# Kernel optimization log

Measured on AMD Instinct MI355X. Metric: run time of the kernel, lower is better.

Reference implementation:

```python
import jax, jax.numpy as jnp
import numpy as np

B, S, D, H = 64, 2048, 512, 512


def setup_inputs() -> dict:
    key = jax.random.key(0)
    ks = jax.random.split(key, 8)
    return {
        "hidden": jax.random.normal(ks[0], (B, D), dtype=jnp.float32),
        "context": jax.random.normal(ks[1], (B, S, D), dtype=jnp.float32),
        "mask": jax.random.randint(ks[2], (B, S), 0, 2).astype(bool),
        "Wd": jax.random.normal(ks[3], (H, D), dtype=jnp.float32) * 0.05,
        "bd": jax.random.normal(ks[4], (H,), dtype=jnp.float32) * 0.05,
        "We": jax.random.normal(ks[5], (H, D), dtype=jnp.float32) * 0.05,
        "be": jax.random.normal(ks[6], (H,), dtype=jnp.float32) * 0.05,
        "V": jax.random.normal(ks[7], (H,), dtype=jnp.float32) * 0.05,
    }


def reference(hidden, context, mask, Wd, bd, We, be, V):
    # di = d_linear(hidden): [B, H]
    di = hidden @ Wd.T + bd
    # ei = e_linear(context): [B, S, H]
    ei = jnp.einsum("bsd,hd->bsh", context, We) + be
    # additive score u_i = V . tanh(di + ei): [B, S]
    ui = jnp.einsum("h,bsh->bs", V, jnp.tanh(di[:, None, :] + ei))
    # masked positions get -inf (ui[mask] = -inf)
    ui = jnp.where(mask, -jnp.inf, ui)
    alpha = jax.nn.softmax(ui, axis=-1)  # [B, S]
    # context aggregation uses the PROJECTED context ei (as in torch code)
    attention_hidden_state = jnp.einsum("bsh,bs->bh", ei, alpha)
    return alpha, attention_hidden_state
```

## Files before the change

kernel.cpp:

```cpp
#include <hip/hip_runtime.h>
#include <cstdint>

#define B_ 64
#define S_ 2048
#define D_ 512
#define H_ 512

using f32x4  = __attribute__((ext_vector_type(4))) float;
using bf16x8 = __attribute__((ext_vector_type(8))) short;

__device__ __forceinline__ unsigned short f2bf(float f) {
  unsigned u = __float_as_uint(f);
  u += 0x7FFFu + ((u >> 16) & 1u);
  return (unsigned short)(u >> 16);
}
__device__ __forceinline__ unsigned int cvtpk(float lo, float hi) {
  unsigned int r;
  asm("v_cvt_pk_bf16_f32 %0, %1, %2" : "=v"(r) : "v"(lo), "v"(hi));
  return r;
}
__device__ __forceinline__ bf16x8 cvt8(f32x4 a, f32x4 b) {
  union { unsigned int u[4]; bf16x8 v; } r;
  r.u[0] = cvtpk(a[0], a[1]); r.u[1] = cvtpk(a[2], a[3]);
  r.u[2] = cvtpk(b[0], b[1]); r.u[3] = cvtpk(b[2], b[3]);
  return r.v;
}
__device__ __forceinline__ float fast_tanh(float x) {
  float t = __builtin_amdgcn_exp2f(x * 2.8853900817779268f);
  return 1.0f - 2.0f * __builtin_amdgcn_rcpf(t + 1.0f);
}

__device__ __forceinline__ void gl_lds16g(const void* g, void* l) {
  __builtin_amdgcn_global_load_lds(
      (const __attribute__((address_space(1))) unsigned int*)g,
      (__attribute__((address_space(3))) unsigned int*)l, 16, 0, 0);
}

__device__ __forceinline__ void barrier_raw() {
  asm volatile("" ::: "memory");
  __builtin_amdgcn_s_barrier();
  asm volatile("" ::: "memory");
}

__global__ void k_prep(const float* __restrict__ hidden, const float* __restrict__ Wd,
                       const float* __restrict__ bd, float* __restrict__ di,
                       const float* __restrict__ We, unsigned short* __restrict__ Web) {
  if (blockIdx.x < 128) {
    int idx = blockIdx.x * 256 + threadIdx.x;
    int h = idx >> 6;
    int b = idx & 63;
    const f32x4* hp = (const f32x4*)(hidden + (size_t)b * D_);
    const f32x4* wp = (const f32x4*)(Wd + (size_t)h * D_);
    float acc = 0.f;
#pragma unroll 8
    for (int i = 0; i < D_ / 4; ++i) {
      f32x4 x = hp[i], y = wp[i];
      acc += x[0] * y[0] + x[1] * y[1] + x[2] * y[2] + x[3] * y[3];
    }
    di[b * H_ + h] = acc + bd[h];
  } else {
    int i = (blockIdx.x - 128) * 256 + threadIdx.x;
    const f32x4* p = (const f32x4*)(We + (size_t)i * 8);
    f32x4 a = p[0], b = p[1];
    bf16x8 o;
    o[0] = (short)f2bf(a[0]); o[1] = (short)f2bf(a[1]);
    o[2] = (short)f2bf(a[2]); o[3] = (short)f2bf(a[3]);
    o[4] = (short)f2bf(b[0]); o[5] = (short)f2bf(b[1]);
    o[6] = (short)f2bf(b[2]); o[7] = (short)f2bf(b[3]);
    *(bf16x8*)(Web + (size_t)i * 8) = o;
  }
}

__global__ __launch_bounds__(512, 2) void k_ei_gemm(
    const float* __restrict__ A, const unsigned short* __restrict__ Bw,
    const float* __restrict__ be, const float* __restrict__ V,
    const float* __restrict__ di, float* __restrict__ ui2) {
  __shared__ __align__(16) float ldsA[2][128 * 32];
  __shared__ __align__(16) unsigned short ldsB[2][256 * 32];
  __shared__ float ured[8][64];

  const int bid = blockIdx.x;
  const int swz = (bid & 7) * 256 + (bid >> 3);
  const int row0 = (swz >> 1) << 7;
  const int nt   = swz & 1;
  const int cb   = nt << 8;

  const int t  = threadIdx.x;
  const int l  = t & 63;
  const int w  = t >> 6;
  const int wm = (w >> 2) << 6;
  const int wn = (w & 3) << 6;
  const int lr = l & 15;
  const int lg = l >> 4;

  const float* gA = A + (size_t)(row0 + w * 8 + (l >> 3)) * D_ +
                    (((l & 7) ^ ((l >> 3) & 7)) << 2);
  const unsigned short* gB = Bw + (size_t)(cb + w * 16 + (l >> 2)) * D_ +
                             (((l & 3) ^ ((l >> 3) & 3)) << 3);

#define STAGE(bf, kk) do {                                     \
    const int k0_ = (kk) << 5;                                 \
    gl_lds16g(gA + k0_,            &ldsA[bf][w * 256]);        \
    gl_lds16g(gA + 64 * D_ + k0_,  &ldsA[bf][2048 + w * 256]); \
    gl_lds16g(gB + k0_,            &ldsB[bf][w * 512]);        \
    gl_lds16g(gB + 128 * D_ + k0_, &ldsB[bf][4096 + w * 512]); \
  } while (0)

  const int pa0 = (((2 * lg)     ^ (lr & 7)) << 2);
  const int pa1 = (((2 * lg + 1) ^ (lr & 7)) << 2);
  const int rsB = (lg ^ ((lr >> 1) & 3)) << 3;
  const int arow = (wm + lr) * 32;
  const int brow = (wn + lr) * 32;

  f32x4 acc[4][4];
  const f32x4 z = {0.f, 0.f, 0.f, 0.f};
#pragma unroll
  for (int mi = 0; mi < 4; ++mi)
#pragma unroll
    for (int ni = 0; ni < 4; ++ni) acc[mi][ni] = z;

  STAGE(0, 0);
  STAGE(1, 1);

#pragma unroll
  for (int kt = 0; kt < 16; ++kt) {
    if (kt == 15) asm volatile("s_waitcnt vmcnt(0)" ::: "memory");
    else          asm volatile("s_waitcnt vmcnt(4)" ::: "memory");
    barrier_raw();
    const int bf = kt & 1;

    bf16x8 bq0 = *(const bf16x8*)&ldsB[bf][brow + 0 * 512 + rsB];
    bf16x8 bq1 = *(const bf16x8*)&ldsB[bf][brow + 1 * 512 + rsB];
    bf16x8 bq2 = *(const bf16x8*)&ldsB[bf][brow + 2 * 512 + rsB];
    bf16x8 bq3 = *(const bf16x8*)&ldsB[bf][brow + 3 * 512 + rsB];

    __builtin_amdgcn_s_setprio(1);
    {
      f32x4 r00 = *(const f32x4*)&ldsA[bf][arow + 0 * 512 + pa0];
      f32x4 r01 = *(const f32x4*)&ldsA[bf][arow + 0 * 512 + pa1];
      f32x4 r10 = *(const f32x4*)&ldsA[bf][arow + 1 * 512 + pa0];
      f32x4 r11 = *(const f32x4*)&ldsA[bf][arow + 1 * 512 + pa1];
      bf16x8 af0 = cvt8(r00, r01);
      bf16x8 af1 = cvt8(r10, r11);
      acc[0][0] = __builtin_amdgcn_mfma_f32_16x16x32_bf16(af0, bq0, acc[0][0], 0, 0, 0);
      acc[0][1] = __builtin_amdgcn_mfma_f32_16x16x32_bf16(af0, bq1, acc[0][1], 0, 0, 0);
      acc[0][2] = __builtin_amdgcn_mfma_f32_16x16x32_bf16(af0, bq2, acc[0][2], 0, 0, 0);
      acc[0][3] = __builtin_amdgcn_mfma_f32_16x16x32_bf16(af0, bq3, acc[0][3], 0, 0, 0);
      acc[1][0] = __builtin_amdgcn_mfma_f32_16x16x32_bf16(af1, bq0, acc[1][0], 0, 0, 0);
      acc[1][1] = __builtin_amdgcn_mfma_f32_16x16x32_bf16(af1, bq1, acc[1][1], 0, 0, 0);
      acc[1][2] = __builtin_amdgcn_mfma_f32_16x16x32_bf16(af1, bq2, acc[1][2], 0, 0, 0);
      acc[1][3] = __builtin_amdgcn_mfma_f32_16x16x32_bf16(af1, bq3, acc[1][3], 0, 0, 0);
    }
    {
      f32x4 r20 = *(const f32x4*)&ldsA[bf][arow + 2 * 512 + pa0];
      f32x4 r21 = *(const f32x4*)&ldsA[bf][arow + 2 * 512 + pa1];
      f32x4 r30 = *(const f32x4*)&ldsA[bf][arow + 3 * 512 + pa0];
      f32x4 r31 = *(const f32x4*)&ldsA[bf][arow + 3 * 512 + pa1];
      bf16x8 af2 = cvt8(r20, r21);
      bf16x8 af3 = cvt8(r30, r31);
      acc[2][0] = __builtin_amdgcn_mfma_f32_16x16x32_bf16(af2, bq0, acc[2][0], 0, 0, 0);
      acc[2][1] = __builtin_amdgcn_mfma_f32_16x16x32_bf16(af2, bq1, acc[2][1], 0, 0, 0);
      acc[2][2] = __builtin_amdgcn_mfma_f32_16x16x32_bf16(af2, bq2, acc[2][2], 0, 0, 0);
      acc[2][3] = __builtin_amdgcn_mfma_f32_16x16x32_bf16(af2, bq3, acc[2][3], 0, 0, 0);
      acc[3][0] = __builtin_amdgcn_mfma_f32_16x16x32_bf16(af3, bq0, acc[3][0], 0, 0, 0);
      acc[3][1] = __builtin_amdgcn_mfma_f32_16x16x32_bf16(af3, bq1, acc[3][1], 0, 0, 0);
      acc[3][2] = __builtin_amdgcn_mfma_f32_16x16x32_bf16(af3, bq2, acc[3][2], 0, 0, 0);
      acc[3][3] = __builtin_amdgcn_mfma_f32_16x16x32_bf16(af3, bq3, acc[3][3], 0, 0, 0);
    }
    __builtin_amdgcn_s_setprio(0);

    __builtin_amdgcn_sched_barrier(0);
    barrier_raw();
    if (kt + 2 < 16) STAGE(bf, kt + 2);
  }
#undef STAGE

  const int b = row0 >> 11;
  float uacc[4][4];
#pragma unroll
  for (int mi = 0; mi < 4; ++mi)
#pragma unroll
    for (int j = 0; j < 4; ++j) uacc[mi][j] = 0.f;

#pragma unroll
  for (int ni = 0; ni < 4; ++ni) {
    const int gc = cb + wn + ni * 16 + lr;
    const float vv = V[gc];
    const float base = di[b * H_ + gc] + be[gc];
#pragma unroll
    for (int mi = 0; mi < 4; ++mi)
#pragma unroll
      for (int j = 0; j < 4; ++j)
        uacc[mi][j] += vv * fast_tanh(base + acc[mi][ni][j]);
  }
#pragma unroll
  for (int mi = 0; mi < 4; ++mi)
#pragma unroll
    for (int j = 0; j < 4; ++j) {
      float s = uacc[mi][j];
      s += __shfl_xor(s, 1);
      s += __shfl_xor(s, 2);
      s += __shfl_xor(s, 4);
      s += __shfl_xor(s, 8);
      if (lr == 0) ured[w][mi * 16 + (lg << 2) + j] = s;
    }
  __syncthreads();
  if (t < 128) {
    const int r = t & 63, wr = t >> 6;
    ui2[nt * (B_ * S_) + row0 + wr * 64 + r] =
        ured[wr * 4][r] + ured[wr * 4 + 1][r] + ured[wr * 4 + 2][r] +
        ured[wr * 4 + 3][r];
  }
}

__global__ void k_softmax(const float* __restrict__ ui2, const void* __restrict__ mask,
                          float* __restrict__ alpha) {
  __shared__ float red[4];
  __shared__ int sfl;
  const int b = blockIdx.x, t = threadIdx.x;
  const int l = t & 63, w = t >> 6;

  if (t == 0) sfl = 0;
  const unsigned int* mw = (const unsigned int*)mask;
  unsigned det = (mw[b * 512 + t] | mw[b * 512 + 256 + t]) & 0xFFFFFF00u;
  __syncthreads();
  if (det) atomicOr(&sfl, 1);
  __syncthreads();
  const int fl = sfl;

  float u[8];
#pragma unroll
  for (int i = 0; i < 8; ++i) {
    const int idx = b * S_ + t + i * 256;
    const int msk = fl ? (int)((const unsigned char*)mask)[idx]
                       : ((const int*)mask)[idx];
    const float uv = ui2[idx] + ui2[idx + B_ * S_];
    u[i] = msk ? -__builtin_inff() : uv;
  }

  float mx = u[0];
#pragma unroll
  for (int i = 1; i < 8; ++i) mx = fmaxf(mx, u[i]);
#pragma unroll
  for (int off = 32; off; off >>= 1) mx = fmaxf(mx, __shfl_xor(mx, off));
  if (l == 0) red[w] = mx;
  __syncthreads();
  mx = fmaxf(fmaxf(red[0], red[1]), fmaxf(red[2], red[3]));
  __syncthreads();

  float p[8];
  float s = 0.f;
#pragma unroll
  for (int i = 0; i < 8; ++i) {
    p[i] = __builtin_amdgcn_exp2f((u[i] - mx) * 1.4426950408889634f);
    s += p[i];
  }
#pragma unroll
  for (int off = 32; off; off >>= 1) s += __shfl_xor(s, off);
  if (l == 0) red[w] = s;
  __syncthreads();
  s = red[0] + red[1] + red[2] + red[3];

  const float inv = 1.0f / s;
#pragma unroll
  for (int i = 0; i < 8; ++i) alpha[b * S_ + t + i * 256] = p[i] * inv;
}

__global__ void k_wsum(const float* __restrict__ ctx, const float* __restrict__ alpha,
                       float* __restrict__ part) {
  __shared__ float red[3][512];
  const int b = blockIdx.x >> 4, chunk = blockIdx.x & 15;
  const int t = threadIdx.x;
  const int h0 = (t & 63) << 3;
  const int sw = t >> 6;
  const int s0 = chunk << 7;

  float acc[8] = {0.f, 0.f, 0.f, 0.f, 0.f, 0.f, 0.f, 0.f};
#pragma unroll 2
  for (int k = 0; k < 32; ++k) {
    const int s = s0 + sw + (k << 2);
    const float a = alpha[b * S_ + s];
    const f32x4* e = (const f32x4*)(ctx + ((size_t)(b * S_ + s)) * D_ + h0);
    f32x4 e0 = e[0], e1 = e[1];
#pragma unroll
    for (int j = 0; j < 4; ++j) acc[j] += a * e0[j];
#pragma unroll
    for (int j = 0; j < 4; ++j) acc[4 + j] += a * e1[j];
  }
  if (sw) {
#pragma unroll
    for (int j = 0; j < 8; ++j) red[sw - 1][h0 + j] = acc[j];
  }
  __syncthreads();
  if (sw == 0) {
#pragma unroll
    for (int j = 0; j < 8; ++j)
      part[((chunk << 6) + b) * 512 + h0 + j] =
          acc[j] + red[0][h0 + j] + red[1][h0 + j] + red[2][h0 + j];
  }
}

__global__ void k_tail(const float* __restrict__ part, const float* __restrict__ We,
                       const float* __restrict__ be, float* __restrict__ out1) {
  __shared__ float wsum_s[512];
  const int b = blockIdx.x, t = threadIdx.x;

  float s = 0.f;
#pragma unroll
  for (int c = 0; c < 16; ++c) s += part[((c << 6) + b) * 512 + t];
  wsum_s[t] = s;
  __syncthreads();

  const f32x4* wp = (const f32x4*)wsum_s;
  const f32x4* ep = (const f32x4*)(We + (size_t)t * D_);
  float acc = 0.f;
#pragma unroll 8
  for (int i = 0; i < D_ / 4; ++i) {
    f32x4 x = wp[i], y = ep[i];
    acc += x[0] * y[0] + x[1] * y[1] + x[2] * y[2] + x[3] * y[3];
  }
  out1[b * H_ + t] = acc + be[t];
}

extern "C" void kernel_launch(void* const* d_in, const int* in_sizes, int n_in,
                              void* d_out, int out_size, void* d_ws, size_t ws_size,
                              hipStream_t stream) {
  const float* hidden = (const float*)d_in[0];
  const float* ctx    = (const float*)d_in[1];
  const void*  mask   = d_in[2];
  const float* Wd     = (const float*)d_in[3];
  const float* bd     = (const float*)d_in[4];
  const float* We     = (const float*)d_in[5];
  const float* be     = (const float*)d_in[6];
  const float* V      = (const float*)d_in[7];

  float* out   = (float*)d_out;
  float* alpha = out;
  float* out1  = out + B_ * S_;

  char* ws = (char*)d_ws;
  const size_t off_u2  = 0;
  const size_t off_r3  = off_u2 + 4ull * B_ * S_ * 4;
  const size_t off_web = off_r3 + (size_t)B_ * H_ * 4;

  float* ui2  = (float*)(ws + off_u2);
  float* part = (float*)(ws + off_u2);
  float* di   = (float*)(ws + off_r3);
  unsigned short* Web = (unsigned short*)(ws + off_web);

  k_prep<<<256, 256, 0, stream>>>(hidden, Wd, bd, di, We, Web);
  k_ei_gemm<<<(B_ * S_ / 128) * 2, 512, 0, stream>>>(ctx, Web, be, V, di, ui2);
  k_softmax<<<B_, 256, 0, stream>>>(ui2, mask, alpha);
  k_wsum<<<B_ * 16, 256, 0, stream>>>(ctx, alpha, part);
  k_tail<<<B_, 512, 0, stream>>>(part, We, be, out1);
}
```

Before: 205.4 us.

## Enlarge GEMM tile to 256 rows, convert A to bf16 once via registers into LDS

Doubles the per-block M tile from 128 to 256 rows and uses a K step of 64. A is now loaded from global memory into registers, converted to bf16 once and written to LDS, instead of being DMA'd as fp32 and converted by every wave on each read. The main loop is restructured into explicit double-buffered phases with many barriers and manual waitcnt control. This halves redundant A conversion and LDS footprint per element and raises reuse of B. In exchange, register pressure rises sharply with 32 accumulators plus 8 staged vectors, occupancy may drop, and the grid shrinks to half as many blocks.

```diff
diff --git a/kernel.cpp b/kernel.cpp
--- a/kernel.cpp
+++ b/kernel.cpp
@@ -8,6 +8,7 @@
 
 using f32x4  = __attribute__((ext_vector_type(4))) float;
 using bf16x8 = __attribute__((ext_vector_type(8))) short;
+using u32x2  = __attribute__((ext_vector_type(2))) unsigned int;
 
 __device__ __forceinline__ unsigned short f2bf(float f) {
   unsigned u = __float_as_uint(f);
@@ -18,12 +19,6 @@
   unsigned int r;
   asm("v_cvt_pk_bf16_f32 %0, %1, %2" : "=v"(r) : "v"(lo), "v"(hi));
   return r;
-}
-__device__ __forceinline__ bf16x8 cvt8(f32x4 a, f32x4 b) {
-  union { unsigned int u[4]; bf16x8 v; } r;
-  r.u[0] = cvtpk(a[0], a[1]); r.u[1] = cvtpk(a[2], a[3]);
-  r.u[2] = cvtpk(b[0], b[1]); r.u[3] = cvtpk(b[2], b[3]);
-  return r.v;
 }
 __device__ __forceinline__ float fast_tanh(float x) {
   float t = __builtin_amdgcn_exp2f(x * 2.8853900817779268f);
@@ -75,110 +70,135 @@
     const float* __restrict__ A, const unsigned short* __restrict__ Bw,
     const float* __restrict__ be, const float* __restrict__ V,
     const float* __restrict__ di, float* __restrict__ ui2) {
-  __shared__ __align__(16) float ldsA[2][128 * 32];
-  __shared__ __align__(16) unsigned short ldsB[2][256 * 32];
-  __shared__ float ured[8][64];
+  __shared__ __align__(16) unsigned short ldsA[2][512 * 32];
+  __shared__ __align__(16) unsigned short ldsB[2][512 * 32];
+  __shared__ float ured[8][128];
 
   const int bid = blockIdx.x;
-  const int swz = (bid & 7) * 256 + (bid >> 3);
-  const int row0 = (swz >> 1) << 7;
+  const int swz = (bid & 7) * 128 + (bid >> 3);
+  const int row0 = (swz >> 1) << 8;
   const int nt   = swz & 1;
   const int cb   = nt << 8;
 
   const int t  = threadIdx.x;
   const int l  = t & 63;
   const int w  = t >> 6;
-  const int wm = (w >> 2) << 6;
+  const int wm = (w >> 2) << 7;
   const int wn = (w & 3) << 6;
   const int lr = l & 15;
   const int lg = l >> 4;
 
-  const float* gA = A + (size_t)(row0 + w * 8 + (l >> 3)) * D_ +
-                    (((l & 7) ^ ((l >> 3) & 7)) << 2);
-  const unsigned short* gB = Bw + (size_t)(cb + w * 16 + (l >> 2)) * D_ +
+  const float* gA = A + (size_t)(row0 + (t >> 4)) * D_ + ((t & 15) << 2);
+  const int khw  = lr >> 3;
+  const int physw = ((lr >> 1) & 3) ^ ((2 * w + (lg >> 1)) & 3);
+  const int eA = ((khw << 8) + (w << 2) + lg) * 32 + (physw << 3) + ((lr & 1) << 2);
+  const unsigned short* gB = Bw + (size_t)(cb + 16 * w + (l >> 2)) * D_ +
                              (((l & 3) ^ ((l >> 3) & 3)) << 3);
-
-#define STAGE(bf, kk) do {                                     \
-    const int k0_ = (kk) << 5;                                 \
-    gl_lds16g(gA + k0_,            &ldsA[bf][w * 256]);        \
-    gl_lds16g(gA + 64 * D_ + k0_,  &ldsA[bf][2048 + w * 256]); \
-    gl_lds16g(gB + k0_,            &ldsB[bf][w * 512]);        \
-    gl_lds16g(gB + 128 * D_ + k0_, &ldsB[bf][4096 + w * 512]); \
+  const int rs = (lg ^ ((lr >> 1) & 3)) << 3;
+
+  f32x4 a0, a1, a2, a3, a4, a5, a6, a7;
+  bf16x8 af[4], bq[4];
+
+#define LOADA(kt) do { const float* p_ = gA + (kt) * 64;                 \
+    a0 = *(const f32x4*)(p_);             a1 = *(const f32x4*)(p_ + 16384);  \
+    a2 = *(const f32x4*)(p_ + 2*16384);   a3 = *(const f32x4*)(p_ + 3*16384);\
+    a4 = *(const f32x4*)(p_ + 4*16384);   a5 = *(const f32x4*)(p_ + 5*16384);\
+    a6 = *(const f32x4*)(p_ + 6*16384);   a7 = *(const f32x4*)(p_ + 7*16384);\
   } while (0)
 
-  const int pa0 = (((2 * lg)     ^ (lr & 7)) << 2);
-  const int pa1 = (((2 * lg + 1) ^ (lr & 7)) << 2);
-  const int rsB = (lg ^ ((lr >> 1) & 3)) << 3;
-  const int arow = (wm + lr) * 32;
-  const int brow = (wn + lr) * 32;
-
-  f32x4 acc[4][4];
+#define WR1(Q, AV, BF) do { u32x2 p_ = {cvtpk(AV[0], AV[1]), cvtpk(AV[2], AV[3])}; \
+    *(u32x2*)&ldsA[BF][eA + (Q) * 1024] = p_; } while (0)
+#define WRITEA(BF) do { WR1(0, a0, BF); WR1(1, a1, BF); WR1(2, a2, BF); \
+    WR1(3, a3, BF); WR1(4, a4, BF); WR1(5, a5, BF); WR1(6, a6, BF);     \
+    WR1(7, a7, BF); } while (0)
+
+#define DMAB(BF, kt) do {                                                    \
+    gl_lds16g(gB + (kt) * 64,                 &ldsB[BF][(16 * w) * 32]);       \
+    gl_lds16g(gB + 128 * D_ + (kt) * 64,      &ldsB[BF][(128 + 16 * w) * 32]); \
+    gl_lds16g(gB + (kt) * 64 + 32,            &ldsB[BF][(256 + 16 * w) * 32]); \
+    gl_lds16g(gB + 128 * D_ + (kt) * 64 + 32, &ldsB[BF][(384 + 16 * w) * 32]); \
+  } while (0)
+
+#define READ_BQ(BF, KH) do { _Pragma("unroll") for (int ni = 0; ni < 4; ++ni) \
+    bq[ni] = *(const bf16x8*)&ldsB[BF][((KH) * 256 + wn + ni * 16 + lr) * 32 + rs]; } while (0)
+#define READ_AF(BF, KH, MH) do { _Pragma("unroll") for (int mi = 0; mi < 4; ++mi) \
+    af[mi] = *(const bf16x8*)&ldsA[BF][((KH) * 256 + wm + (MH) * 64 + mi * 16 + lr) * 32 + rs]; } while (0)
+
+#define MFMA16(MH) do {                                                  \
+    __builtin_amdgcn_s_setprio(1);                                       \
+    _Pragma("unroll") for (int mi = 0; mi < 4; ++mi)                     \
+      _Pragma("unroll") for (int ni = 0; ni < 4; ++ni)                   \
+        acc[(MH) * 4 + mi][ni] = __builtin_amdgcn_mfma_f32_16x16x32_bf16(\
+            af[mi], bq[ni], acc[(MH) * 4 + mi][ni], 0, 0, 0);            \
+    __builtin_amdgcn_s_setprio(0);                                       \
+  } while (0)
+
+#define VMW8 asm volatile("s_waitcnt lgkmcnt(0)\n\ts_waitcnt vmcnt(8)" ::: "memory")
+#define VMW0 asm volatile("s_waitcnt lgkmcnt(0)\n\ts_waitcnt vmcnt(0)" ::: "memory")
+
+  f32x4 acc[8][4];
   const f32x4 z = {0.f, 0.f, 0.f, 0.f};
 #pragma unroll
-  for (int mi = 0; mi < 4; ++mi)
+  for (int mi = 0; mi < 8; ++mi)
 #pragma unroll
     for (int ni = 0; ni < 4; ++ni) acc[mi][ni] = z;
 
-  STAGE(0, 0);
-  STAGE(1, 1);
-
-#pragma unroll
-  for (int kt = 0; kt < 16; ++kt) {
-    if (kt == 15) asm volatile("s_waitcnt vmcnt(0)" ::: "memory");
-    else          asm volatile("s_waitcnt vmcnt(4)" ::: "memory");
-    barrier_raw();
-    const int bf = kt & 1;
-
-    bf16x8 bq0 = *(const bf16x8*)&ldsB[bf][brow + 0 * 512 + rsB];
-    bf16x8 bq1 = *(const bf16x8*)&ldsB[bf][brow + 1 * 512 + rsB];
-    bf16x8 bq2 = *(const bf16x8*)&ldsB[bf][brow + 2 * 512 + rsB];
-    bf16x8 bq3 = *(const bf16x8*)&ldsB[bf][brow + 3 * 512 + rsB];
-
-    __builtin_amdgcn_s_setprio(1);
-    {
-      f32x4 r00 = *(const f32x4*)&ldsA[bf][arow + 0 * 512 + pa0];
-      f32x4 r01 = *(const f32x4*)&ldsA[bf][arow + 0 * 512 + pa1];
-      f32x4 r10 = *(const f32x4*)&ldsA[bf][arow + 1 * 512 + pa0];
-      f32x4 r11 = *(const f32x4*)&ldsA[bf][arow + 1 * 512 + pa1];
-      bf16x8 af0 = cvt8(r00, r01);
-      bf16x8 af1 = cvt8(r10, r11);
-      acc[0][0] = __builtin_amdgcn_mfma_f32_16x16x32_bf16(af0, bq0, acc[0][0], 0, 0, 0);
-      acc[0][1] = __builtin_amdgcn_mfma_f32_16x16x32_bf16(af0, bq1, acc[0][1], 0, 0, 0);
-      acc[0][2] = __builtin_amdgcn_mfma_f32_16x16x32_bf16(af0, bq2, acc[0][2], 0, 0, 0);
-      acc[0][3] = __builtin_amdgcn_mfma_f32_16x16x32_bf16(af0, bq3, acc[0][3], 0, 0, 0);
-      acc[1][0] = __builtin_amdgcn_mfma_f32_16x16x32_bf16(af1, bq0, acc[1][0], 0, 0, 0);
-      acc[1][1] = __builtin_amdgcn_mfma_f32_16x16x32_bf16(af1, bq1, acc[1][1], 0, 0, 0);
-      acc[1][2] = __builtin_amdgcn_mfma_f32_16x16x32_bf16(af1, bq2, acc[1][2], 0, 0, 0);
-      acc[1][3] = __builtin_amdgcn_mfma_f32_16x16x32_bf16(af1, bq3, acc[1][3], 0, 0, 0);
-    }
-    {
-      f32x4 r20 = *(const f32x4*)&ldsA[bf][arow + 2 * 512 + pa0];
-      f32x4 r21 = *(const f32x4*)&ldsA[bf][arow + 2 * 512 + pa1];
-      f32x4 r30 = *(const f32x4*)&ldsA[bf][arow + 3 * 512 + pa0];
-      f32x4 r31 = *(const f32x4*)&ldsA[bf][arow + 3 * 512 + pa1];
-      bf16x8 af2 = cvt8(r20, r21);
-      bf16x8 af3 = cvt8(r30, r31);
-      acc[2][0] = __builtin_amdgcn_mfma_f32_16x16x32_bf16(af2, bq0, acc[2][0], 0, 0, 0);
-      acc[2][1] = __builtin_amdgcn_mfma_f32_16x16x32_bf16(af2, bq1, acc[2][1], 0, 0, 0);
-      acc[2][2] = __builtin_amdgcn_mfma_f32_16x16x32_bf16(af2, bq2, acc[2][2], 0, 0, 0);
-      acc[2][3] = __builtin_amdgcn_mfma_f32_16x16x32_bf16(af2, bq3, acc[2][3], 0, 0, 0);
-      acc[3][0] = __builtin_amdgcn_mfma_f32_16x16x32_bf16(af3, bq0, acc[3][0], 0, 0, 0);
-      acc[3][1] = __builtin_amdgcn_mfma_f32_16x16x32_bf16(af3, bq1, acc[3][1], 0, 0, 0);
-      acc[3][2] = __builtin_amdgcn_mfma_f32_16x16x32_bf16(af3, bq2, acc[3][2], 0, 0, 0);
-      acc[3][3] = __builtin_amdgcn_mfma_f32_16x16x32_bf16(af3, bq3, acc[3][3], 0, 0, 0);
-    }
-    __builtin_amdgcn_s_setprio(0);
-
-    __builtin_amdgcn_sched_barrier(0);
-    barrier_raw();
-    if (kt + 2 < 16) STAGE(bf, kt + 2);
-  }
-#undef STAGE
+  LOADA(0);
+  DMAB(0, 0);
+  WRITEA(0);
+  LOADA(1);
+  VMW8;
+  barrier_raw();
+
+#define ITER(I, LASTQ)                                                        \
+  do {                                                                        \
+                     \
+    READ_BQ(0, 0); READ_AF(0, 0, 0);                                          \
+    DMAB(1, 2 * (I) + 1);                                                     \
+    WRITEA(1);                                                                \
+    if (!(LASTQ)) LOADA(2 * (I) + 2);                                         \
+    barrier_raw(); MFMA16(0); barrier_raw();                                  \
+                                                          \
+    READ_AF(0, 0, 1); barrier_raw(); MFMA16(1); barrier_raw();                \
+                                                          \
+    READ_BQ(0, 1); READ_AF(0, 1, 0); barrier_raw(); MFMA16(0); barrier_raw(); \
+                                     \
+    READ_AF(0, 1, 1); barrier_raw(); MFMA16(1);                               \
+    if (LASTQ) { VMW0; } else { VMW8; }                                       \
+    barrier_raw();                                                            \
+                     \
+    READ_BQ(1, 0); READ_AF(1, 0, 0);                                          \
+    if (!(LASTQ)) { DMAB(0, 2 * (I) + 2); WRITEA(0); LOADA(2 * (I) + 3); }    \
+    barrier_raw(); MFMA16(0); barrier_raw();                                  \
+                                                          \
+    READ_AF(1, 0, 1); barrier_raw(); MFMA16(1); barrier_raw();                \
+                                                          \
+    READ_BQ(1, 1); READ_AF(1, 1, 0); barrier_raw(); MFMA16(0); barrier_raw(); \
+                                     \
+    READ_AF(1, 1, 1); barrier_raw(); MFMA16(1);                               \
+    if (LASTQ) { VMW0; } else { VMW8; }                                       \
+    barrier_raw();                                                            \
+  } while (0)
+
+  ITER(0, 0);
+  ITER(1, 0);
+  ITER(2, 0);
+  ITER(3, 1);
+#undef ITER
+#undef LOADA
+#undef WR1
+#undef WRITEA
+#undef DMAB
+#undef READ_BQ
+#undef READ_AF
+#undef MFMA16
+#undef VMW8
+#undef VMW0
 
   const int b = row0 >> 11;
-  float uacc[4][4];
-#pragma unroll
-  for (int mi = 0; mi < 4; ++mi)
+  float uacc[8][4];
+#pragma unroll
+  for (int mi = 0; mi < 8; ++mi)
 #pragma unroll
     for (int j = 0; j < 4; ++j) uacc[mi][j] = 0.f;
 
@@ -188,13 +208,13 @@
     const float vv = V[gc];
     const float base = di[b * H_ + gc] + be[gc];
 #pragma unroll
-    for (int mi = 0; mi < 4; ++mi)
+    for (int mi = 0; mi < 8; ++mi)
 #pragma unroll
       for (int j = 0; j < 4; ++j)
         uacc[mi][j] += vv * fast_tanh(base + acc[mi][ni][j]);
   }
 #pragma unroll
-  for (int mi = 0; mi < 4; ++mi)
+  for (int mi = 0; mi < 8; ++mi)
 #pragma unroll
     for (int j = 0; j < 4; ++j) {
       float s = uacc[mi][j];
@@ -205,11 +225,11 @@
       if (lr == 0) ured[w][mi * 16 + (lg << 2) + j] = s;
     }
   __syncthreads();
-  if (t < 128) {
-    const int r = t & 63, wr = t >> 6;
-    ui2[nt * (B_ * S_) + row0 + wr * 64 + r] =
-        ured[wr * 4][r] + ured[wr * 4 + 1][r] + ured[wr * 4 + 2][r] +
-        ured[wr * 4 + 3][r];
+  if (t < 256) {
+    const int half = t >> 7, r = t & 127;
+    ui2[nt * (B_ * S_) + row0 + half * 128 + r] =
+        ured[half * 4][r] + ured[half * 4 + 1][r] + ured[half * 4 + 2][r] +
+        ured[half * 4 + 3][r];
   }
 }
 
@@ -349,7 +369,7 @@
   unsigned short* Web = (unsigned short*)(ws + off_web);
 
   k_prep<<<256, 256, 0, stream>>>(hidden, Wd, bd, di, We, Web);
-  k_ei_gemm<<<(B_ * S_ / 128) * 2, 512, 0, stream>>>(ctx, Web, be, V, di, ui2);
+  k_ei_gemm<<<(B_ * S_ / 256) * 2, 512, 0, stream>>>(ctx, Web, be, V, di, ui2);
   k_softmax<<<B_, 256, 0, stream>>>(ui2, mask, alpha);
   k_wsum<<<B_ * 16, 256, 0, stream>>>(ctx, alpha, part);
   k_tail<<<B_, 512, 0, stream>>>(part, We, be, out1);
```

After: 267.2 us. 1.3x slower.
